# Performance work log

Hardware: AMD Instinct MI355X
Metric: run time of the kernel (lower is better)

Reference implementation:

```python
import jax, jax.numpy as jnp
import numpy as np

K_TABLE = 8388608   # number of stored key/value pairs (2**23)
N_QUERY = 4194304   # number of lookups (2**22)
KEY_SPACE = 2147483647
DEFAULT_VALUE = -1  # DenseHashTable default_value for missing keys


def setup_inputs() -> dict:
    key = jax.random.key(0)
    k1, k2, k3, k4 = jax.random.split(key, 4)
    # Hash table contents, represented as a sorted key array + aligned values.
    table_keys = jnp.sort(jax.random.randint(k1, (K_TABLE,), 1, KEY_SPACE, dtype=jnp.int64))
    table_values = jax.random.randint(k2, (K_TABLE,), 0, 1000000, dtype=jnp.int64)
    # Queries: half random ids (mostly misses), half sampled from the table (hits).
    q_rand = jax.random.randint(k3, (N_QUERY // 2,), 1, KEY_SPACE, dtype=jnp.int64)
    hit_idx = jax.random.randint(k4, (N_QUERY // 2,), 0, K_TABLE, dtype=jnp.int64)
    q_hit = table_keys[hit_idx]
    query = jnp.concatenate([q_rand, q_hit])
    return {"query": query, "table_keys": table_keys, "table_values": table_values}


def reference(query, table_keys, table_values):
    # DenseHashTable.lookup: for each query id return its stored value,
    # or default_value (-1) if the key is absent. Implemented as a sorted
    # binary-search gather (same math: exact-match key -> value map).
    idx = jnp.searchsorted(table_keys, query)                 # [N]
    idx_c = jnp.clip(idx, 0, table_keys.shape[0] - 1)
    hit = table_keys[idx_c] == query                          # [N] bool
    out = jnp.where(hit, table_values[idx_c], jnp.int64(DEFAULT_VALUE))
    return out
```

## Files before the change

### kernel.cpp

```cpp
#include <hip/hip_runtime.h>


constexpr int WCAP = 1024;
constexpr int NBLK = 1 << 15;

__device__ __forceinline__ int lower_bound_u(const int* __restrict__ keys,
                                             int lo, int hi, unsigned t) {
    while (lo < hi) {
        int m = (lo + hi) >> 1;
        if ((unsigned)keys[m] < t) lo = m + 1; else hi = m;
    }
    return lo;
}

__global__ void block_index_kernel(const int* __restrict__ keys, int K,
                                   int* __restrict__ bstart) {
    int i = blockIdx.x * blockDim.x + threadIdx.x;
    if (i > NBLK) return;
    bstart[i] = lower_bound_u(keys, 0, K, ((unsigned)i) << 16);
}

__global__ void __launch_bounds__(256) build_packed3_kernel(
        const int* __restrict__ keys, const int* __restrict__ vals, int K,
        const int* __restrict__ bstart, int4* __restrict__ table) {
    __shared__ int s_keys[WCAP];
    __shared__ int s_vals[WCAP];
    int wlo = bstart[blockIdx.x];
    int whi = bstart[blockIdx.x + 1];
    int wn = whi - wlo;
    bool use_lds = (wn <= WCAP);
    if (use_lds) {
        for (int j = threadIdx.x; j < wn; j += 256) {
            s_keys[j] = keys[wlo + j];
            s_vals[j] = vals[wlo + j];
        }
    }
    __syncthreads();

    unsigned b = (unsigned)blockIdx.x * 256u + threadIdx.x;
    unsigned tlo = b << 8;
    unsigned thi = tlo + 256u;

    int w[4] = {0, 0, 0, 0};
    bool ok = true;
    int cnt = 0;
    int lo_global;

    if (use_lds) {
        int l = 0, h = wn;
        while (l < h) {
            int m = (l + h) >> 1;
            if ((unsigned)s_keys[m] < tlo) l = m + 1; else h = m;
        }
        lo_global = wlo + l;
        int j = l;
        while (j < wn && (unsigned)s_keys[j] < thi) {
            if (cnt >= 4) { ok = false; break; }
            int v = s_vals[j];
            if ((unsigned)v > 0xFFFFFu) { ok = false; break; }
            w[cnt] = (1 << 28) | (v << 8) | (s_keys[j] & 0xFF);
            ++cnt; ++j;
        }
    } else {
        int l = lower_bound_u(keys, wlo, whi, tlo);
        lo_global = l;
        int j = l;
        while (j < whi && (unsigned)keys[j] < thi) {
            if (cnt >= 4) { ok = false; break; }
            int v = vals[j];
            if ((unsigned)v > 0xFFFFFu) { ok = false; break; }
            w[cnt] = (1 << 28) | (v << 8) | (keys[j] & 0xFF);
            ++cnt; ++j;
        }
    }
    table[b] = ok ? make_int4(w[0], w[1], w[2], w[3])
                  : make_int4(2 << 28, lo_global, 0, 0);
}

__device__ __forceinline__ int resolve_packed(int q, int4 e,
                                              const int* __restrict__ keys,
                                              const int* __restrict__ vals,
                                              int K) {
    if ((((unsigned)e.x) >> 28) == 2u) {
        for (int j = e.y; j < K; ++j) {
            int k = keys[j];
            if ((unsigned)k >= (unsigned)q) return (k == q) ? vals[j] : -1;
        }
        return -1;
    }
    int ql = q & 0xFF;
    int w;
    w = e.x; if ((((unsigned)w) >> 28) == 1u && (w & 0xFF) == ql) return (w >> 8) & 0xFFFFF;
    w = e.y; if ((((unsigned)w) >> 28) == 1u && (w & 0xFF) == ql) return (w >> 8) & 0xFFFFF;
    w = e.z; if ((((unsigned)w) >> 28) == 1u && (w & 0xFF) == ql) return (w >> 8) & 0xFFFFF;
    w = e.w; if ((((unsigned)w) >> 28) == 1u && (w & 0xFF) == ql) return (w >> 8) & 0xFFFFF;
    return -1;
}

__global__ void lookup_packed_kernel(const int* __restrict__ query,
                                     const int* __restrict__ keys,
                                     const int* __restrict__ vals,
                                     const int4* __restrict__ table,
                                     int* __restrict__ out,
                                     int N, int K, unsigned Bmask) {
    int half = (N + 1) >> 1;
    int i = blockIdx.x * blockDim.x + threadIdx.x;
    if (i >= half) return;
    int i1 = i + half;
    bool has1 = (i1 < N);
    int q0 = query[i];
    int q1 = has1 ? query[i1] : q0;
    int4 e0 = table[(((unsigned)q0) >> 8) & Bmask];
    int4 e1 = table[(((unsigned)q1) >> 8) & Bmask];
    out[i] = resolve_packed(q0, e0, keys, vals, K);
    if (has1) out[i1] = resolve_packed(q1, e1, keys, vals, K);
}

__global__ void lookup_bsearch_kernel(const int* __restrict__ query,
                                      const int* __restrict__ keys,
                                      const int* __restrict__ vals,
                                      int* __restrict__ out,
                                      int N, int K) {
    int i = blockIdx.x * blockDim.x + threadIdx.x;
    if (i >= N) return;
    int q = query[i];
    int lo = lower_bound_u(keys, 0, K, (unsigned)q);
    int r = -1;
    if (lo < K && keys[lo] == q) r = vals[lo];
    out[i] = r;
}

extern "C" void kernel_launch(void* const* d_in, const int* in_sizes, int n_in,
                              void* d_out, int out_size, void* d_ws, size_t ws_size,
                              hipStream_t stream) {
    const int* query = (const int*)d_in[0];
    const int* keys  = (const int*)d_in[1];
    const int* vals  = (const int*)d_in[2];
    int* out = (int*)d_out;
    const int N = in_sizes[0];
    const int K = in_sizes[1];
    const int tb = 256;

    const size_t TABLE_BYTES = (size_t)16 << 23;
    const size_t IDX_BYTES   = (size_t)(NBLK + 1) * 4;

    if (TABLE_BYTES <= ws_size) {
        const unsigned B = 1u << 23;
        int4* table = (int4*)d_ws;
        int* bstart = (TABLE_BYTES + IDX_BYTES <= ws_size)
                          ? (int*)((char*)d_ws + TABLE_BYTES)
                          : (int*)d_out;
        block_index_kernel<<<(NBLK + 1 + tb - 1) / tb, tb, 0, stream>>>(keys, K, bstart);
        build_packed3_kernel<<<NBLK, tb, 0, stream>>>(keys, vals, K, bstart, table);
        int half = (N + 1) >> 1;
        lookup_packed_kernel<<<(half + tb - 1) / tb, tb, 0, stream>>>(
            query, keys, vals, table, out, N, K, B - 1);
    } else {
        lookup_bsearch_kernel<<<(N + tb - 1) / tb, tb, 0, stream>>>(query, keys,
                                                                    vals, out, N, K);
    }
}
```

Measured before the change: 163.4 us.

## Build packed bucket table by key-parallel rank scatter instead of per-bucket search

The build kernel stops having each thread binary-search its bucket in LDS and walk the keys. Instead, each thread handles keys: it marks the first key of each bucket, computes each key's rank within its bucket, and scatters the packed entries into a shared per-bucket array, with an overflow flag that falls back to a scan start. This removes the per-thread binary search and the divergent walks, at the cost of two extra barriers and about 6KB more shared memory per block, which can reduce occupancy. Buckets with no keys read s_first without it being set, but the flag is 0 for them, so s_first is never used.

After: 136.0 us. 1.2x faster.

```diff
diff --git a/kernel.cpp b/kernel.cpp
--- a/kernel.cpp
+++ b/kernel.cpp
@@ -20,51 +20,66 @@
     bstart[i] = lower_bound_u(keys, 0, K, ((unsigned)i) << 16);
 }
 
-__global__ void __launch_bounds__(256) build_packed3_kernel(
+__global__ void __launch_bounds__(256) build_rank_kernel(
         const int* __restrict__ keys, const int* __restrict__ vals, int K,
         const int* __restrict__ bstart, int4* __restrict__ table) {
     __shared__ int s_keys[WCAP];
     __shared__ int s_vals[WCAP];
-    int wlo = bstart[blockIdx.x];
-    int whi = bstart[blockIdx.x + 1];
-    int wn = whi - wlo;
-    bool use_lds = (wn <= WCAP);
-    if (use_lds) {
-        for (int j = threadIdx.x; j < wn; j += 256) {
+    __shared__ int s_first[256];
+    __shared__ int s_flag[256];
+    __shared__ int s_ent[256][4];
+
+    const int tid = threadIdx.x;
+    const int wlo = bstart[blockIdx.x];
+    const int whi = bstart[blockIdx.x + 1];
+    const int wn = whi - wlo;
+    const unsigned base_b = (unsigned)blockIdx.x << 8;
+
+    s_flag[tid] = 0;
+    s_ent[tid][0] = 0; s_ent[tid][1] = 0; s_ent[tid][2] = 0; s_ent[tid][3] = 0;
+
+    if (wn <= WCAP) {
+        for (int j = tid; j < wn; j += 256) {
             s_keys[j] = keys[wlo + j];
             s_vals[j] = vals[wlo + j];
         }
-    }
-    __syncthreads();
+        __syncthreads();
 
-    unsigned b = (unsigned)blockIdx.x * 256u + threadIdx.x;
-    unsigned tlo = b << 8;
-    unsigned thi = tlo + 256u;
+        for (int j = tid; j < wn; j += 256) {
+            unsigned b = ((unsigned)s_keys[j]) >> 8;
+            bool first = (j == 0) || ((((unsigned)s_keys[j - 1]) >> 8) != b);
+            if (first) s_first[b & 255u] = j;
+        }
+        __syncthreads();
 
-    int w[4] = {0, 0, 0, 0};
-    bool ok = true;
-    int cnt = 0;
-    int lo_global;
+        for (int j = tid; j < wn; j += 256) {
+            int k = s_keys[j];
+            unsigned lb = (((unsigned)k) >> 8) & 255u;
+            int rank = j - s_first[lb];
+            int v = s_vals[j];
+            if (rank < 4 && (unsigned)v <= 0xFFFFFu) {
+                s_ent[lb][rank] = (1 << 28) | (v << 8) | (k & 0xFF);
+            } else {
+                s_flag[lb] = 1;
+            }
+        }
+        __syncthreads();
 
-    if (use_lds) {
-        int l = 0, h = wn;
-        while (l < h) {
-            int m = (l + h) >> 1;
-            if ((unsigned)s_keys[m] < tlo) l = m + 1; else h = m;
-        }
-        lo_global = wlo + l;
-        int j = l;
-        while (j < wn && (unsigned)s_keys[j] < thi) {
-            if (cnt >= 4) { ok = false; break; }
-            int v = s_vals[j];
-            if ((unsigned)v > 0xFFFFFu) { ok = false; break; }
-            w[cnt] = (1 << 28) | (v << 8) | (s_keys[j] & 0xFF);
-            ++cnt; ++j;
-        }
+        int4 e;
+        if (s_flag[tid]) e = make_int4(2 << 28, wlo + s_first[tid], 0, 0);
+        else             e = make_int4(s_ent[tid][0], s_ent[tid][1],
+                                       s_ent[tid][2], s_ent[tid][3]);
+        table[base_b + tid] = e;
     } else {
-        int l = lower_bound_u(keys, wlo, whi, tlo);
-        lo_global = l;
-        int j = l;
+        __syncthreads();
+        unsigned b = base_b + tid;
+        unsigned tlo = b << 8;
+        unsigned thi = tlo + 256u;
+        int lo = lower_bound_u(keys, wlo, whi, tlo);
+        int w[4] = {0, 0, 0, 0};
+        bool ok = true;
+        int cnt = 0;
+        int j = lo;
         while (j < whi && (unsigned)keys[j] < thi) {
             if (cnt >= 4) { ok = false; break; }
             int v = vals[j];
@@ -72,9 +87,9 @@
             w[cnt] = (1 << 28) | (v << 8) | (keys[j] & 0xFF);
             ++cnt; ++j;
         }
+        table[b] = ok ? make_int4(w[0], w[1], w[2], w[3])
+                      : make_int4(2 << 28, lo, 0, 0);
     }
-    table[b] = ok ? make_int4(w[0], w[1], w[2], w[3])
-                  : make_int4(2 << 28, lo_global, 0, 0);
 }
 
 __device__ __forceinline__ int resolve_packed(int q, int4 e,
@@ -123,10 +138,10 @@
                                       int N, int K) {
     int i = blockIdx.x * blockDim.x + threadIdx.x;
     if (i >= N) return;
-    int q = query[i];
-    int lo = lower_bound_u(keys, 0, K, (unsigned)q);
+    unsigned q = (unsigned)query[i];
+    int lo = lower_bound_u(keys, 0, K, q);
     int r = -1;
-    if (lo < K && keys[lo] == q) r = vals[lo];
+    if (lo < K && (unsigned)keys[lo] == q) r = vals[lo];
     out[i] = r;
 }
 
@@ -151,7 +166,7 @@
                           ? (int*)((char*)d_ws + TABLE_BYTES)
                           : (int*)d_out;
         block_index_kernel<<<(NBLK + 1 + tb - 1) / tb, tb, 0, stream>>>(keys, K, bstart);
-        build_packed3_kernel<<<NBLK, tb, 0, stream>>>(keys, vals, K, bstart, table);
+        build_rank_kernel<<<NBLK, tb, 0, stream>>>(keys, vals, K, bstart, table);
         int half = (N + 1) >> 1;
         lookup_packed_kernel<<<(half + tb - 1) / tb, tb, 0, stream>>>(
             query, keys, vals, table, out, N, K, B - 1);
```
